# Optimization experiments

Hardware: AMD Instinct MI355X
Metric: run time of the kernel (lower is better)

The kernel has to match this reference:

```python
import jax, jax.numpy as jnp
import numpy as np

# dims
B, H, W = 2, 128, 256
MD = 34            # model_dim (last 2 channels = sin/cos lat)
LD = MD - 2        # learnable_dim = 32
NH, HD = 4, 8      # n_heads, head_dim
SH = 64            # shared_hidden (DISCO out channels)
K = 25             # number of DISCO basis functions (5x5 kernel_shape)
P = 7              # local stencil width (lat x lon support of geodesic basis)
R = P // 2
FF1, FF2 = 512, 256


def setup_inputs() -> dict:
    key = jax.random.key(0)
    ks = jax.random.split(key, 16)
    x = jax.random.normal(ks[0], (B, H, W, MD), dtype=jnp.float32)
    # latitude-dependent sparse geodesic basis values over a 7x7 stencil
    psi_val = jax.random.uniform(ks[1], (K, H, P * P), dtype=jnp.float32) * 0.1
    disco_w = jax.random.normal(ks[2], (SH, K), dtype=jnp.float32) * 0.1
    disco_b = jax.random.normal(ks[3], (SH,), dtype=jnp.float32) * 0.01
    # per-head MLP: shared_hidden -> 32 -> 1
    hw1 = jax.random.normal(ks[4], (NH, SH, 32), dtype=jnp.float32) * (1.0 / np.sqrt(SH))
    hb1 = jax.random.normal(ks[5], (NH, 32), dtype=jnp.float32) * 0.01
    hw2 = jax.random.normal(ks[6], (NH, 32, 1), dtype=jnp.float32) * (1.0 / np.sqrt(32))
    hb2 = jax.random.normal(ks[7], (NH, 1), dtype=jnp.float32) * 0.01
    # FFN: model_dim -> 512 -> 256 -> learnable_dim
    fw1 = jax.random.normal(ks[8], (MD, FF1), dtype=jnp.float32) * (1.0 / np.sqrt(MD))
    fw1 = fw1.at[-2:, :].set(0.0)  # matches ffn[0].weight[:, -2:] = 0 init
    fb1 = jax.random.normal(ks[9], (FF1,), dtype=jnp.float32) * 0.01
    fw2 = jax.random.normal(ks[10], (FF1, FF2), dtype=jnp.float32) * (1.0 / np.sqrt(FF1))
    fb2 = jax.random.normal(ks[11], (FF2,), dtype=jnp.float32) * 0.01
    fw3 = jax.random.normal(ks[12], (FF2, LD), dtype=jnp.float32) * (1.0 / np.sqrt(FF2))
    fb3 = jax.random.normal(ks[13], (LD,), dtype=jnp.float32) * 0.01
    return {"x": x, "psi_val": psi_val, "disco_w": disco_w, "disco_b": disco_b,
            "hw1": hw1, "hb1": hb1, "hw2": hw2, "hb2": hb2,
            "fw1": fw1, "fb1": fb1, "fw2": fw2, "fb2": fb2, "fw3": fw3, "fb3": fb3}


def _gelu(t):
    return jax.nn.gelu(t, approximate=False)  # torch nn.GELU default (erf)


def _disco_s2(xn, psi_val, disco_w, disco_b):
    """DISCO sparse-basis conv on single-channel maps.
    xn: (N, H, W). Basis values vary with output latitude, longitude is
    translation-invariant; support is a lat-clamped / lon-wrapped 7x7 stencil.
    Returns (N, SH, H, W)."""
    xp = jnp.pad(xn, ((0, 0), (R, R), (0, 0)), mode="edge")  # clamp at poles
    shifts = []
    for dlat in range(P):
        row = xp[:, dlat:dlat + H, :]
        for dlon in range(-R, R + 1):
            shifts.append(jnp.roll(row, -dlon, axis=2))  # wrap in longitude
    xs = jnp.stack(shifts, axis=1)  # (N, P*P, H, W)
    basis = jnp.einsum("khp,nphw->nkhw", psi_val, xs)       # basis aggregation
    return jnp.einsum("fk,nkhw->nfhw", disco_w, basis) + disco_b[None, :, None, None]


def reference(x, psi_val, disco_w, disco_b, hw1, hb1, hw2, hb2,
              fw1, fb1, fw2, fb2, fw3, fb3):
    x_learn = x[..., :LD]
    sin_cos = x[..., LD:]
    x_res = x_learn
    # (B,H,W,LD) -> (B*LD, H, W): each learnable channel is a 1-channel map
    xn = x_learn.transpose(0, 3, 1, 2).reshape(B * LD, H, W)
    d = _disco_s2(xn, psi_val, disco_w, disco_b)              # (B*LD, SH, H, W)
    d = d.reshape(B, LD, SH, H, W).transpose(0, 3, 4, 1, 2)    # (B,H,W,LD,SH)
    # per-head MLP over its head_dim slice (head index is outer in LD)
    d = d.reshape(B, H, W, NH, HD, SH)
    h = _gelu(jnp.einsum("bxynds,nso->bxyndo", d, hw1) + hb1[None, None, None, :, None, :])
    h = jnp.einsum("bxyndo,noe->bxynde", h, hw2) + hb2[None, None, None, :, None, :]
    x_learn = h[..., 0].reshape(B, H, W, LD)
    x_learn = x_learn + x_res                                  # use_residual
    x_full = jnp.concatenate([x_learn, sin_cos], axis=-1)
    x_res2 = x_learn
    t = _gelu(x_full @ fw1 + fb1)
    t = _gelu(t @ fw2 + fb2)
    t = t @ fw3 + fb3                                          # dropout p=0 -> id
    x_learn = t + x_res2
    return jnp.concatenate([x_learn, sin_cos], axis=-1)
```

## Files before the change

kernel.cpp:

```cpp
#include <hip/hip_runtime.h>
#include <math.h>


typedef __attribute__((ext_vector_type(8))) short bfrag;
typedef __attribute__((ext_vector_type(4))) float ffrag;
typedef __attribute__((ext_vector_type(4))) short short4v;

union bfi4 { int4 i; bfrag b; };

__device__ __forceinline__ float gelu_f(float v) {
  const float z = v * (2.3022077484f + 0.1029451564f * v * v);
  const float e = __builtin_amdgcn_exp2f(-z);
  return v * __builtin_amdgcn_rcpf(1.0f + e);
}

__device__ __forceinline__ short f2bf(float f) {
  union { float f; unsigned u; } v; v.f = f;
  unsigned r = (v.u + 0x7fffu + ((v.u >> 16) & 1u)) >> 16;
  return (short)r;
}

__device__ __forceinline__ short f2bf_fast(float f) {
  union { float f; unsigned u; } v; v.f = f;
  return (short)((v.u + 0x8000u) >> 16);
}

__device__ __forceinline__ float bf2f(short s) {
  union { float f; unsigned u; } v;
  v.u = ((unsigned)(unsigned short)s) << 16;
  return v.f;
}

__device__ __forceinline__ int pkbf(float a, float b) {
  union { float f; unsigned u; } va, vb; va.f = a; vb.f = b;
  return (int)__builtin_amdgcn_perm(vb.u + 0x8000u, va.u + 0x8000u, 0x07060302u);
}

template <int CTRL>
__device__ __forceinline__ float dpp_add(float v) {
  union { float f; int i; } s, t;
  s.f = v;
  t.i = __builtin_amdgcn_update_dpp(0, s.i, CTRL, 0xf, 0xf, true);
  return v + t.f;
}
__device__ __forceinline__ float reduce16(float v) {
  v = dpp_add<0xB1>(v);
  v = dpp_add<0x4E>(v);
  v = dpp_add<0x141>(v);
  v = dpp_add<0x140>(v);
  return v;
}

__device__ __forceinline__ void st4bf(short* p, float4 v) {
  short4v s;
  s[0] = f2bf(v.x); s[1] = f2bf(v.y); s[2] = f2bf(v.z); s[3] = f2bf(v.w);
  *(short4v*)p = s;
}

__global__ __launch_bounds__(256) void k01_prep(
    const float* __restrict__ psi, const float* __restrict__ dw,
    const float* __restrict__ db,
    const float* __restrict__ fw1, const float* __restrict__ fw2,
    const float* __restrict__ fw3, const float* __restrict__ hw1,
    const float* __restrict__ hb1,
    short* __restrict__ wcb, short* __restrict__ fw1s,
    short* __restrict__ fw2s, short* __restrict__ fw3s,
    short* __restrict__ hw1b, float* __restrict__ hb1e) {
  __shared__ __align__(16) char sm[33280];
  const int bid = blockIdx.x;
  const int tid = threadIdx.x;

  if (bid < 128) {
    short* tile = (short*)sm;
    const int h = bid;
    const int lane = tid & 63;
    const int w = __builtin_amdgcn_readfirstlane(tid >> 6);
    float dwreg[25];
#pragma unroll
    for (int kk = 0; kk < 25; ++kk) dwreg[kk] = dw[lane * 25 + kk];
    const int p0 = w * 13;
    const int pend = (p0 + 13 < 49) ? (p0 + 13) : 49;
#pragma unroll 1
    for (int p = p0; p < pend; ++p) {
      float acc = 0.f;
#pragma unroll
      for (int kk = 0; kk < 25; ++kk)
        acc += dwreg[kk] * psi[kk * 6272 + h * 49 + p];
      tile[lane * 52 + p] = f2bf(acc);
    }
    __syncthreads();
    short* outp = wcb + h * 8192;
    for (int idx = tid; idx < 8192; idx += 256) {
      const int jj = idx & 7, ln = (idx >> 3) & 63;
      const int nt = (idx >> 9) & 3, kt = (idx >> 11) & 1, par = idx >> 12;
      const int k = kt * 32 + (ln >> 4) * 8 + jj;
      const int f = nt * 16 + (ln & 15);
      const int r = k >> 3, dlt = k & 7;
      const int j = par ? (dlt - 1) : dlt;
      short v = 0;
      if (r < 7 && j >= 0 && j < 7) v = tile[f * 52 + r * 7 + j];
      outp[idx] = v;
    }
    return;
  }

  if (bid < 144) {
    short* S = (short*)sm;
    const int kt = bid - 128;
    const float* src = fw2 + kt * 8192;
    for (int q = tid; q < 2048; q += 256) {
      const int lin = q * 4;
      const int kk = lin >> 8, nn = lin & 255;
      st4bf(S + kk * 260 + nn, *(const float4*)(src + lin));
    }
    __syncthreads();
    short* dst = fw2s + kt * 8192;
    for (int q = tid; q < 8192; q += 256) {
      const int jj = q & 7, lane = (q >> 3) & 63, nt = q >> 9;
      const int kk = (lane >> 4) * 8 + jj, nn = nt * 16 + (lane & 15);
      dst[q] = S[kk * 260 + nn];
    }
    return;
  }

  if (bid == 144) {
    short* S = (short*)sm;
    for (int q = tid; q < 4096; q += 256) {
      const int lin = q * 4;
      const int kk = lin >> 9, nn = lin & 511;
      st4bf(S + kk * 516 + nn, *(const float4*)(fw1 + lin));
    }
    __syncthreads();
    for (int q = tid; q < 16384; q += 256) {
      const int jj = q & 7, lane = (q >> 3) & 63, nt = q >> 9;
      const int kk = (lane >> 4) * 8 + jj, nn = nt * 16 + (lane & 15);
      fw1s[q] = S[kk * 516 + nn];
    }
    return;
  }

  if (bid == 145) {
    short* S = (short*)sm;
    for (int q = tid; q < 2048; q += 256) {
      const int lin = q * 4;
      const int kk = lin >> 5, nn = lin & 31;
      st4bf(S + kk * 36 + nn, *(const float4*)(fw3 + lin));
    }
    __syncthreads();
    for (int q = tid; q < 8192; q += 256) {
      const int jj = q & 7, lane = (q >> 3) & 63;
      const int nt = (q >> 9) & 1, kt = q >> 10;
      const int kk = kt * 32 + (lane >> 4) * 8 + jj, nn = nt * 16 + (lane & 15);
      fw3s[q] = S[kk * 36 + nn];
    }
    return;
  }

  if (bid == 146) {
    short* S = (short*)sm;
    for (int q = tid; q < 2048; q += 256) {
      const int lin = q * 4;
      const int row = lin >> 5, nn = lin & 31;
      st4bf(S + row * 36 + nn, *(const float4*)(hw1 + lin));
    }
    __syncthreads();
    for (int q = tid; q < 8192; q += 256) {
      const int jj = q & 7, lane = (q >> 3) & 63;
      const int fr = (q >> 9) & 3, hd = q >> 11;
      const int kt = fr >> 1, nt = fr & 1;
      const int s = kt * 32 + (lane >> 4) * 8 + jj;
      const int forig = (s & 3) * 16 + (s >> 2);
      const int o = nt * 16 + (lane & 15);
      hw1b[q] = S[(hd * 64 + forig) * 36 + o];
    }
    return;
  }

  if (tid < 128) {
    const int n = tid >> 5, o = tid & 31;
    float acc = hb1[n * 32 + o];
#pragma unroll
    for (int s = 0; s < 64; ++s)
      acc += hw1[n * 2048 + s * 32 + o] * db[s];
    hb1e[tid] = acc;
  }
}

__global__ __launch_bounds__(256, 4) void k23_fused(
    const float* __restrict__ x,    const short* __restrict__ wcb,
    const short* __restrict__ hw1b, const float* __restrict__ hb1e,
    const float* __restrict__ hw2,  const float* __restrict__ hb2,
    const short* __restrict__ fw1s, const short* __restrict__ fw2s,
    const short* __restrict__ fw3s,
    const float* __restrict__ fb1,  const float* __restrict__ fb2,
    const float* __restrict__ fb3,  float* __restrict__ outb) {
  __shared__ __align__(16) char smem[36224];
  short* sX = (short*)smem;
  short* sM = (short*)(smem + 34048);

  const int tid = threadIdx.x;
  const int w0  = blockIdx.x * 32;
  const int h   = blockIdx.y;
  const int b   = blockIdx.z;

  {
    int4* p = (int4*)sX;
    int4 z; z.x = z.y = z.z = z.w = 0;
    for (int e = tid; e < (32 * 388) / 8; e += 256) p[e] = z;
  }
  __syncthreads();

#pragma unroll 1
  for (int r = 0; r < 7; ++r) {
    int hr = h - 3 + r; hr = hr < 0 ? 0 : (hr > 127 ? 127 : hr);
    const float* __restrict__ xrow = x + (size_t)((b * 128 + hr) * 256) * 34;
    short* __restrict__ sxr = sX + r * 48;
    for (int e = tid; e < 39 * 16; e += 256) {
      const int c2 = e & 15;
      const int wp = e >> 4;
      const int wr = (w0 - 3 + wp) & 255;
      const float2 v = *(const float2*)&xrow[wr * 34 + c2 * 2];
      short* dp = sxr + (c2 * 2) * 388 + wp;
      dp[0]   = f2bf_fast(v.x);
      dp[388] = f2bf_fast(v.y);
    }
  }

  if (tid < 64) {
    const int wl = tid >> 1;
    const int sc = tid & 1;
    const int idx = ((b * 128 + h) * 256 + (w0 + wl)) * 34 + 32 + sc;
    outb[idx] = x[idx];
  }
  __syncthreads();

  const int lane = tid & 63, lm = lane & 15, lq = lane >> 4;
  const int n = tid >> 6;

  float hb1v[2], hw2v[2];
#pragma unroll
  for (int nt = 0; nt < 2; ++nt) {
    hb1v[nt] = hb1e[n * 32 + nt * 16 + lm];
    hw2v[nt] = hw2[n * 32 + nt * 16 + lm];
  }
  const float hb2n = hb2[n];

  bfrag cB[2][2][4];
#pragma unroll
  for (int par = 0; par < 2; ++par)
#pragma unroll
    for (int kt = 0; kt < 2; ++kt)
#pragma unroll
      for (int nt = 0; nt < 4; ++nt)
        cB[par][kt][nt] = *(const bfrag*)(wcb + h * 8192 +
                            ((par * 2 + kt) * 4 + nt) * 512 + lane * 8);
  bfrag mB[2][2];
#pragma unroll
  for (int kt = 0; kt < 2; ++kt)
#pragma unroll
    for (int nt = 0; nt < 2; ++nt)
      mB[kt][nt] = *(const bfrag*)(hw1b + n * 2048 + (kt * 2 + nt) * 512 + lane * 8);

  short* sDw = (short*)(smem + 24832) + n * 1152;
  const int* tpB = (const int*)sX;

#pragma unroll 1
  for (int i = 0; i < 8; ++i) {
    const int c = n * 8 + i;

    const int base0 = c * 194 + lq * 24 + lm;
    bfi4 u0, u1;
    u0.i.x = tpB[base0];      u0.i.y = tpB[base0 + 1];
    u0.i.z = tpB[base0 + 2];  u0.i.w = tpB[base0 + 3];
    u1.i.x = tpB[base0 + 96]; u1.i.y = tpB[base0 + 97];
    u1.i.z = tpB[base0 + 98]; u1.i.w = tpB[base0 + 99];

#pragma unroll
    for (int par = 0; par < 2; ++par) {
      ffrag dacc[4];
#pragma unroll
      for (int nt = 0; nt < 4; ++nt) dacc[nt] = ffrag{0.f, 0.f, 0.f, 0.f};
#pragma unroll
      for (int nt = 0; nt < 4; ++nt) {
        dacc[nt] = __builtin_amdgcn_mfma_f32_16x16x32_bf16(u0.b, cB[par][0][nt], dacc[nt], 0, 0, 0);
        dacc[nt] = __builtin_amdgcn_mfma_f32_16x16x32_bf16(u1.b, cB[par][1][nt], dacc[nt], 0, 0, 0);
      }

#pragma unroll
      for (int rr = 0; rr < 4; ++rr) {
        int2 w;
        w.x = pkbf(dacc[0][rr], dacc[1][rr]);
        w.y = pkbf(dacc[2][rr], dacc[3][rr]);
        *(int2*)(sDw + (lq * 4 + rr) * 72 + lm * 4) = w;
      }

      bfrag a10 = *(const bfrag*)(sDw + lm * 72 + lq * 8);
      bfrag a11 = *(const bfrag*)(sDw + lm * 72 + 32 + lq * 8);
      ffrag h10 = {0.f, 0.f, 0.f, 0.f}, h11 = {0.f, 0.f, 0.f, 0.f};
      h10 = __builtin_amdgcn_mfma_f32_16x16x32_bf16(a10, mB[0][0], h10, 0, 0, 0);
      h10 = __builtin_amdgcn_mfma_f32_16x16x32_bf16(a11, mB[1][0], h10, 0, 0, 0);
      h11 = __builtin_amdgcn_mfma_f32_16x16x32_bf16(a10, mB[0][1], h11, 0, 0, 0);
      h11 = __builtin_amdgcn_mfma_f32_16x16x32_bf16(a11, mB[1][1], h11, 0, 0, 0);

#pragma unroll
      for (int rr = 0; rr < 4; ++rr) {
        float v = gelu_f(h10[rr] + hb1v[0]) * hw2v[0] +
                  gelu_f(h11[rr] + hb1v[1]) * hw2v[1];
        v = reduce16(v);
        const int p = 2 * (lq * 4 + rr) + par;
        const float res = bf2f(sX[c * 388 + 144 + 3 + p]);
        if (lm == 0) sM[p * 34 + c] = f2bf_fast(v + hb2n + res);
      }
    }
  }
  __syncthreads();

  short* sT1h = (short*)smem;
  short* sT2  = (short*)(smem + 16896);
  const int wave = n;
  const int koff = lq * 8;
  const int mt3 = wave & 1;
  const int nt3 = wave >> 1;
  const int col3 = nt3 * 16 + lm;
  const int pixg = (b * 128 + h) * 256 + w0;

  bfrag aF[2];
#pragma unroll
  for (int mt = 0; mt < 2; ++mt)
    aF[mt] = *(const bfrag*)(sM + (mt * 16 + lm) * 34 + koff);
  float res3[4];
#pragma unroll
  for (int r = 0; r < 4; ++r)
    res3[r] = bf2f(sM[(mt3 * 16 + lq * 4 + r) * 34 + col3]);

  const int n0 = wave * 4;
  ffrag acc[2][4];
#pragma unroll
  for (int mt = 0; mt < 2; ++mt)
#pragma unroll
    for (int ni = 0; ni < 4; ++ni) acc[mt][ni] = ffrag{0.f, 0.f, 0.f, 0.f};
  const short* w2base = fw2s + n0 * 512 + lane * 8;

#pragma unroll 1
  for (int H = 0; H < 2; ++H) {
    bfrag b1f[4];
#pragma unroll
    for (int ni = 0; ni < 4; ++ni)
      b1f[ni] = *(const bfrag*)(fw1s + (H * 16 + wave * 4 + ni) * 512 + lane * 8);
#pragma unroll
    for (int ni = 0; ni < 4; ++ni) {
      const int ntl = wave * 4 + ni;
#pragma unroll
      for (int mt = 0; mt < 2; ++mt) {
        ffrag cc = {0.f, 0.f, 0.f, 0.f};
        cc = __builtin_amdgcn_mfma_f32_16x16x32_bf16(aF[mt], b1f[ni], cc, 0, 0, 0);
        const int colg = H * 256 + ntl * 16 + lm;
        const float bias = fb1[colg];
#pragma unroll
        for (int r = 0; r < 4; ++r) {
          const int row = mt * 16 + lq * 4 + r;
          sT1h[row * 264 + ntl * 16 + lm] = f2bf_fast(gelu_f(cc[r] + bias));
        }
      }
    }
    __syncthreads();

#pragma unroll 2
    for (int kt = 0; kt < 8; ++kt) {
      bfrag bv[4];
#pragma unroll
      for (int ni = 0; ni < 4; ++ni)
        bv[ni] = *(const bfrag*)(w2base + (H * 8 + kt) * 8192 + ni * 512);
      const bfrag a0 = *(const bfrag*)(sT1h + lm * 264 + kt * 32 + koff);
      const bfrag a1 = *(const bfrag*)(sT1h + (16 + lm) * 264 + kt * 32 + koff);
#pragma unroll
      for (int ni = 0; ni < 4; ++ni) {
        acc[0][ni] = __builtin_amdgcn_mfma_f32_16x16x32_bf16(a0, bv[ni], acc[0][ni], 0, 0, 0);
        acc[1][ni] = __builtin_amdgcn_mfma_f32_16x16x32_bf16(a1, bv[ni], acc[1][ni], 0, 0, 0);
      }
    }
    __syncthreads();
  }

#pragma unroll
  for (int mt = 0; mt < 2; ++mt)
#pragma unroll
    for (int ni = 0; ni < 4; ++ni) {
      const int col = (n0 + ni) * 16 + lm;
      const float bias = fb2[col];
#pragma unroll
      for (int r = 0; r < 4; ++r) {
        const int row = mt * 16 + lq * 4 + r;
        sT2[row * 264 + col] = f2bf_fast(gelu_f(acc[mt][ni][r] + bias));
      }
    }
  __syncthreads();

  ffrag c3 = {0.f, 0.f, 0.f, 0.f};
  const short* sA3 = sT2 + (mt3 * 16 + lm) * 264 + koff;
#pragma unroll
  for (int kt = 0; kt < 8; ++kt) {
    const bfrag a = *(const bfrag*)(sA3 + kt * 32);
    const bfrag bw = *(const bfrag*)(fw3s + nt3 * 512 + kt * 1024 + lane * 8);
    c3 = __builtin_amdgcn_mfma_f32_16x16x32_bf16(a, bw, c3, 0, 0, 0);
  }
  {
    const float bias = fb3[col3];
#pragma unroll
    for (int r = 0; r < 4; ++r) {
      const int row = mt3 * 16 + lq * 4 + r;
      outb[(pixg + row) * 34 + col3] = c3[r] + bias + res3[r];
    }
  }
}

extern "C" void kernel_launch(void* const* d_in, const int* in_sizes, int n_in,
                              void* d_out, int out_size, void* d_ws, size_t ws_size,
                              hipStream_t stream) {
  const float* x   = (const float*)d_in[0];
  const float* psi = (const float*)d_in[1];
  const float* dw  = (const float*)d_in[2];
  const float* db  = (const float*)d_in[3];
  const float* hw1 = (const float*)d_in[4];
  const float* hb1 = (const float*)d_in[5];
  const float* hw2 = (const float*)d_in[6];
  const float* hb2 = (const float*)d_in[7];
  const float* fw1 = (const float*)d_in[8];
  const float* fb1 = (const float*)d_in[9];
  const float* fw2 = (const float*)d_in[10];
  const float* fb2 = (const float*)d_in[11];
  const float* fw3 = (const float*)d_in[12];
  const float* fb3 = (const float*)d_in[13];
  float* outb = (float*)d_out;

  short* wcb  = (short*)d_ws;
  short* fw1s = wcb + 1048576;
  short* fw2s = fw1s + 16384;
  short* fw3s = fw2s + 131072;
  short* hw1b = fw3s + 8192;
  float* hb1e = (float*)(hw1b + 8192);

  hipLaunchKernelGGL(k01_prep, dim3(148), dim3(256), 0, stream,
                     psi, dw, db, fw1, fw2, fw3, hw1, hb1,
                     wcb, fw1s, fw2s, fw3s, hw1b, hb1e);
  hipLaunchKernelGGL(k23_fused, dim3(8, 128, 2), dim3(256), 0, stream,
                     x, wcb, hw1b, hb1e, hw2, hb2,
                     fw1s, fw2s, fw3s, fb1, fb2, fb3, outb);
}
```

Baseline: 172.6 us.

## Fold per-head MLP first layer into DISCO stencil weights per latitude

The prep kernel now precomposes the head MLP's first-layer weights (hw1) with the latitude-dependent DISCO stencil weights. Each latitude row therefore gets a direct stencil-to-hidden weight matrix for each head. The fused kernel drops the intermediate 64-channel DISCO output, its LDS round trip and the second MFMA stage, and runs one MFMA pair per head straight from the input patch. This also shrinks LDS, allowing launch bounds to rise to 6 blocks per CU. The cost is a workspace weight table twice as large (per-head weights per latitude), extra prep arithmetic, and bf16 rounding of the combined weights instead of the separate ones.

```diff
diff --git a/kernel.cpp b/kernel.cpp
--- a/kernel.cpp
+++ b/kernel.cpp
@@ -29,11 +29,6 @@
   union { float f; unsigned u; } v;
   v.u = ((unsigned)(unsigned short)s) << 16;
   return v.f;
-}
-
-__device__ __forceinline__ int pkbf(float a, float b) {
-  union { float f; unsigned u; } va, vb; va.f = a; vb.f = b;
-  return (int)__builtin_amdgcn_perm(vb.u + 0x8000u, va.u + 0x8000u, 0x07060302u);
 }
 
 template <int CTRL>
@@ -65,16 +60,22 @@
     const float* __restrict__ hb1,
     short* __restrict__ wcb, short* __restrict__ fw1s,
     short* __restrict__ fw2s, short* __restrict__ fw3s,
-    short* __restrict__ hw1b, float* __restrict__ hb1e) {
-  __shared__ __align__(16) char sm[33280];
+    float* __restrict__ hb1e) {
+  __shared__ __align__(16) char sm[59392];
   const int bid = blockIdx.x;
   const int tid = threadIdx.x;
 
   if (bid < 128) {
-    short* tile = (short*)sm;
+    float* tileL = (float*)sm;
+    short* tile2 = (short*)(sm + 13312);
+    float* hw1L  = (float*)(sm + 26624);
     const int h = bid;
     const int lane = tid & 63;
     const int w = __builtin_amdgcn_readfirstlane(tid >> 6);
+
+    for (int e = tid; e < 2048; e += 256)
+      ((float4*)hw1L)[e] = ((const float4*)hw1)[e];
+
     float dwreg[25];
 #pragma unroll
     for (int kk = 0; kk < 25; ++kk) dwreg[kk] = dw[lane * 25 + kk];
@@ -86,19 +87,40 @@
 #pragma unroll
       for (int kk = 0; kk < 25; ++kk)
         acc += dwreg[kk] * psi[kk * 6272 + h * 49 + p];
-      tile[lane * 52 + p] = f2bf(acc);
-    }
-    __syncthreads();
-    short* outp = wcb + h * 8192;
-    for (int idx = tid; idx < 8192; idx += 256) {
+      tileL[lane * 52 + p] = acc;
+    }
+    __syncthreads();
+
+    for (int e = tid; e < 4096; e += 256) {
+      const int no = e >> 5, pp = e & 31;
+      if (pp < 25) {
+        const int p2 = pp * 2;
+        const int nn = no >> 5, o = no & 31;
+        const float* hp = hw1L + nn * 2048 + o;
+        float a0 = 0.f, a1 = 0.f;
+#pragma unroll 4
+        for (int f = 0; f < 64; ++f) {
+          const float wv = hp[f * 32];
+          a0 += wv * tileL[f * 52 + p2];
+          a1 += wv * tileL[f * 52 + p2 + 1];
+        }
+        tile2[no * 52 + p2] = f2bf(a0);
+        if (p2 + 1 < 49) tile2[no * 52 + p2 + 1] = f2bf(a1);
+      }
+    }
+    __syncthreads();
+
+    short* outp = wcb + h * 16384;
+    for (int idx = tid; idx < 16384; idx += 256) {
       const int jj = idx & 7, ln = (idx >> 3) & 63;
-      const int nt = (idx >> 9) & 3, kt = (idx >> 11) & 1, par = idx >> 12;
-      const int k = kt * 32 + (ln >> 4) * 8 + jj;
-      const int f = nt * 16 + (ln & 15);
+      const int nt = (idx >> 9) & 1, kt = (idx >> 10) & 1;
+      const int par = (idx >> 11) & 1, nn = idx >> 12;
+      const int k = kt * 32 + ((ln >> 4) << 3) + jj;
+      const int o = nt * 16 + (ln & 15);
       const int r = k >> 3, dlt = k & 7;
       const int j = par ? (dlt - 1) : dlt;
       short v = 0;
-      if (r < 7 && j >= 0 && j < 7) v = tile[f * 52 + r * 7 + j];
+      if (r < 7 && j >= 0 && j < 7) v = tile2[(nn * 32 + o) * 52 + r * 7 + j];
       outp[idx] = v;
     }
     return;
@@ -156,26 +178,6 @@
     return;
   }
 
-  if (bid == 146) {
-    short* S = (short*)sm;
-    for (int q = tid; q < 2048; q += 256) {
-      const int lin = q * 4;
-      const int row = lin >> 5, nn = lin & 31;
-      st4bf(S + row * 36 + nn, *(const float4*)(hw1 + lin));
-    }
-    __syncthreads();
-    for (int q = tid; q < 8192; q += 256) {
-      const int jj = q & 7, lane = (q >> 3) & 63;
-      const int fr = (q >> 9) & 3, hd = q >> 11;
-      const int kt = fr >> 1, nt = fr & 1;
-      const int s = kt * 32 + (lane >> 4) * 8 + jj;
-      const int forig = (s & 3) * 16 + (s >> 2);
-      const int o = nt * 16 + (lane & 15);
-      hw1b[q] = S[(hd * 64 + forig) * 36 + o];
-    }
-    return;
-  }
-
   if (tid < 128) {
     const int n = tid >> 5, o = tid & 31;
     float acc = hb1[n * 32 + o];
@@ -186,17 +188,17 @@
   }
 }
 
-__global__ __launch_bounds__(256, 4) void k23_fused(
+__global__ __launch_bounds__(256, 6) void k23_fused(
     const float* __restrict__ x,    const short* __restrict__ wcb,
-    const short* __restrict__ hw1b, const float* __restrict__ hb1e,
-    const float* __restrict__ hw2,  const float* __restrict__ hb2,
+    const float* __restrict__ hb1e, const float* __restrict__ hw2,
+    const float* __restrict__ hb2,
     const short* __restrict__ fw1s, const short* __restrict__ fw2s,
     const short* __restrict__ fw3s,
     const float* __restrict__ fb1,  const float* __restrict__ fb2,
     const float* __restrict__ fb3,  float* __restrict__ outb) {
-  __shared__ __align__(16) char smem[36224];
+  __shared__ __align__(16) char smem[27008];
   short* sX = (short*)smem;
-  short* sM = (short*)(smem + 34048);
+  short* sM = (short*)(smem + 24832);
 
   const int tid = threadIdx.x;
   const int w0  = blockIdx.x * 32;
@@ -245,23 +247,16 @@
   }
   const float hb2n = hb2[n];
 
-  bfrag cB[2][2][4];
+  bfrag cW[2][2][2];
 #pragma unroll
   for (int par = 0; par < 2; ++par)
 #pragma unroll
     for (int kt = 0; kt < 2; ++kt)
 #pragma unroll
-      for (int nt = 0; nt < 4; ++nt)
-        cB[par][kt][nt] = *(const bfrag*)(wcb + h * 8192 +
-                            ((par * 2 + kt) * 4 + nt) * 512 + lane * 8);
-  bfrag mB[2][2];
-#pragma unroll
-  for (int kt = 0; kt < 2; ++kt)
-#pragma unroll
-    for (int nt = 0; nt < 2; ++nt)
-      mB[kt][nt] = *(const bfrag*)(hw1b + n * 2048 + (kt * 2 + nt) * 512 + lane * 8);
-
-  short* sDw = (short*)(smem + 24832) + n * 1152;
+      for (int nt = 0; nt < 2; ++nt)
+        cW[par][kt][nt] = *(const bfrag*)(wcb + h * 16384 + n * 4096 +
+                            ((par * 2 + kt) * 2 + nt) * 512 + lane * 8);
+
   const int* tpB = (const int*)sX;
 
 #pragma unroll 1
@@ -277,35 +272,16 @@
 
 #pragma unroll
     for (int par = 0; par < 2; ++par) {
-      ffrag dacc[4];
-#pragma unroll
-      for (int nt = 0; nt < 4; ++nt) dacc[nt] = ffrag{0.f, 0.f, 0.f, 0.f};
-#pragma unroll
-      for (int nt = 0; nt < 4; ++nt) {
-        dacc[nt] = __builtin_amdgcn_mfma_f32_16x16x32_bf16(u0.b, cB[par][0][nt], dacc[nt], 0, 0, 0);
-        dacc[nt] = __builtin_amdgcn_mfma_f32_16x16x32_bf16(u1.b, cB[par][1][nt], dacc[nt], 0, 0, 0);
-      }
+      ffrag h0 = {0.f, 0.f, 0.f, 0.f}, h1 = {0.f, 0.f, 0.f, 0.f};
+      h0 = __builtin_amdgcn_mfma_f32_16x16x32_bf16(u0.b, cW[par][0][0], h0, 0, 0, 0);
+      h0 = __builtin_amdgcn_mfma_f32_16x16x32_bf16(u1.b, cW[par][1][0], h0, 0, 0, 0);
+      h1 = __builtin_amdgcn_mfma_f32_16x16x32_bf16(u0.b, cW[par][0][1], h1, 0, 0, 0);
+      h1 = __builtin_amdgcn_mfma_f32_16x16x32_bf16(u1.b, cW[par][1][1], h1, 0, 0, 0);
 
 #pragma unroll
       for (int rr = 0; rr < 4; ++rr) {
-        int2 w;
-        w.x = pkbf(dacc[0][rr], dacc[1][rr]);
-        w.y = pkbf(dacc[2][rr], dacc[3][rr]);
-        *(int2*)(sDw + (lq * 4 + rr) * 72 + lm * 4) = w;
-      }
-
-      bfrag a10 = *(const bfrag*)(sDw + lm * 72 + lq * 8);
-      bfrag a11 = *(const bfrag*)(sDw + lm * 72 + 32 + lq * 8);
-      ffrag h10 = {0.f, 0.f, 0.f, 0.f}, h11 = {0.f, 0.f, 0.f, 0.f};
-      h10 = __builtin_amdgcn_mfma_f32_16x16x32_bf16(a10, mB[0][0], h10, 0, 0, 0);
-      h10 = __builtin_amdgcn_mfma_f32_16x16x32_bf16(a11, mB[1][0], h10, 0, 0, 0);
-      h11 = __builtin_amdgcn_mfma_f32_16x16x32_bf16(a10, mB[0][1], h11, 0, 0, 0);
-      h11 = __builtin_amdgcn_mfma_f32_16x16x32_bf16(a11, mB[1][1], h11, 0, 0, 0);
-
-#pragma unroll
-      for (int rr = 0; rr < 4; ++rr) {
-        float v = gelu_f(h10[rr] + hb1v[0]) * hw2v[0] +
-                  gelu_f(h11[rr] + hb1v[1]) * hw2v[1];
+        float v = gelu_f(h0[rr] + hb1v[0]) * hw2v[0] +
+                  gelu_f(h1[rr] + hb1v[1]) * hw2v[1];
         v = reduce16(v);
         const int p = 2 * (lq * 4 + rr) + par;
         const float res = bf2f(sX[c * 388 + 144 + 3 + p]);
@@ -316,7 +292,7 @@
   __syncthreads();
 
   short* sT1h = (short*)smem;
-  short* sT2  = (short*)(smem + 16896);
+  short* sT2  = (short*)smem;
   const int wave = n;
   const int koff = lq * 8;
   const int mt3 = wave & 1;
@@ -434,16 +410,15 @@
   float* outb = (float*)d_out;
 
   short* wcb  = (short*)d_ws;
-  short* fw1s = wcb + 1048576;
+  short* fw1s = wcb + 2097152;
   short* fw2s = fw1s + 16384;
   short* fw3s = fw2s + 131072;
-  short* hw1b = fw3s + 8192;
-  float* hb1e = (float*)(hw1b + 8192);
-
-  hipLaunchKernelGGL(k01_prep, dim3(148), dim3(256), 0, stream,
+  float* hb1e = (float*)(fw3s + 8192);
+
+  hipLaunchKernelGGL(k01_prep, dim3(147), dim3(256), 0, stream,
                      psi, dw, db, fw1, fw2, fw3, hw1, hb1,
-                     wcb, fw1s, fw2s, fw3s, hw1b, hb1e);
+                     wcb, fw1s, fw2s, fw3s, hb1e);
   hipLaunchKernelGGL(k23_fused, dim3(8, 128, 2), dim3(256), 0, stream,
-                     x, wcb, hw1b, hb1e, hw2, hb2,
+                     x, wcb, hb1e, hw2, hb2,
                      fw1s, fw2s, fw3s, fb1, fb2, fb3, outb);
 }
```

After: 198.2 us. 14.8% more time.
